# Kernel optimization log

Hardware: AMD Instinct MI355X
Metric: run time of the kernel (lower is better)

## Reference

```python
import jax, jax.numpy as jnp
import numpy as np

B, Q, C, V = 512, 100, 81, 117  # batch, queries, obj classes (80+no-object), verbs
THRES, ALPHA, BETA = 0.7, 1.0, 0.5


def setup_inputs() -> dict:
    key = jax.random.key(0)
    k1, k2, k3, k4, k5, k6 = jax.random.split(key, 6)
    out_obj_logits = jax.random.normal(k1, (B, Q, C), jnp.float32)
    out_verb_logits = jax.random.normal(k2, (B, Q, V), jnp.float32)
    out_sub_boxes = jax.random.uniform(k3, (B, Q, 4), jnp.float32)
    out_obj_boxes = jax.random.uniform(k4, (B, Q, 4), jnp.float32)
    # correct_mat: binary verb-object compatibility [V, C-1] + ones column for no-object slot -> [V, C]
    cm = (jax.random.uniform(k5, (V, C - 1)) < 0.3).astype(jnp.float32)
    correct_mat = jnp.concatenate([cm, jnp.ones((V, 1), jnp.float32)], axis=1)
    target_sizes = jax.random.randint(k6, (B, 2), 480, 1334).astype(jnp.int64)
    return {
        'out_obj_logits': out_obj_logits,
        'out_verb_logits': out_verb_logits,
        'out_sub_boxes': out_sub_boxes,
        'out_obj_boxes': out_obj_boxes,
        'correct_mat': correct_mat,
        'target_sizes': target_sizes,
    }


def _box_cxcywh_to_xyxy(b):
    cx, cy, w, h = b[..., 0], b[..., 1], b[..., 2], b[..., 3]
    return jnp.stack([cx - 0.5 * w, cy - 0.5 * h, cx + 0.5 * w, cy + 0.5 * h], axis=-1)


def _pairwise_iou(boxes):  # boxes [Q,4] xyxy (pixel coords, +1 convention as in source)
    x1, y1, x2, y2 = boxes[:, 0], boxes[:, 1], boxes[:, 2], boxes[:, 3]
    area = (x2 - x1 + 1.0) * (y2 - y1 + 1.0)
    xx1 = jnp.maximum(x1[:, None], x1[None, :])
    yy1 = jnp.maximum(y1[:, None], y1[None, :])
    xx2 = jnp.minimum(x2[:, None], x2[None, :])
    yy2 = jnp.minimum(y2[:, None], y2[None, :])
    w = jnp.maximum(0.0, xx2 - xx1 + 1.0)
    h = jnp.maximum(0.0, yy2 - yy1 + 1.0)
    inter = w * h
    union = area[:, None] + area[None, :] - inter
    return inter / union


def _nms_one_image(sub_b, obj_b, obj_lab, max_scores):
    # Greedy pairwise triplet NMS. Grouping key in the source degenerates to the
    # object label alone (subject cat is constant, verb-label string identical),
    # so suppression applies only between detections with the same object label.
    order = jnp.argsort(-max_scores)
    sb, ob, lab = sub_b[order], obj_b[order], obj_lab[order]
    ovr = jnp.power(_pairwise_iou(sb), ALPHA) * jnp.power(_pairwise_iou(ob), BETA)
    upper = jnp.triu(jnp.ones((Q, Q), bool), 1)
    sup_mat = upper & (lab[:, None] == lab[None, :]) & (ovr > THRES)

    def body(i, supp):
        return supp | (sup_mat[i] & jnp.logical_not(supp[i]))

    supp = jax.lax.fori_loop(0, Q, body, jnp.zeros((Q,), bool))
    keep = jnp.zeros((Q,), bool).at[order].set(jnp.logical_not(supp))
    return keep  # in original query order


def reference(out_obj_logits, out_verb_logits, out_sub_boxes, out_obj_boxes, correct_mat, target_sizes):
    obj_prob = jax.nn.softmax(out_obj_logits, axis=-1)
    obj_scores = obj_prob[..., :-1].max(axis=-1)            # [B,Q]
    obj_labels = obj_prob[..., :-1].argmax(axis=-1)         # [B,Q]
    verb_scores = jax.nn.sigmoid(out_verb_logits)           # [B,Q,V]

    ts = target_sizes.astype(jnp.float32)
    img_h, img_w = ts[:, 0], ts[:, 1]
    scale_fct = jnp.stack([img_w, img_h, img_w, img_h], axis=1)  # [B,4]
    sub_boxes = _box_cxcywh_to_xyxy(out_sub_boxes) * scale_fct[:, None, :]
    obj_boxes = _box_cxcywh_to_xyxy(out_obj_boxes) * scale_fct[:, None, :]

    # masks[b,q,v] = correct_mat[v, obj_labels[b,q]]
    masks = correct_mat.T[obj_labels]                        # [B,Q,V]
    hoi_scores = verb_scores * obj_scores[..., None] * masks

    max_scores = hoi_scores.max(axis=-1)                     # [B,Q]
    keep = jax.vmap(_nms_one_image)(sub_boxes, obj_boxes, obj_labels, max_scores)
    return hoi_scores, obj_labels, sub_boxes, obj_boxes, keep
```

## Files before the change

kernel.cpp:

```cpp
#include <hip/hip_runtime.h>
#include <math.h>

#define Bn 512
#define Qn 100
#define Cn 81
#define Vn 117
#define NQ (Bn * Qn)

#define OFF_HOI  0
#define OFF_LAB  (NQ * Vn)
#define OFF_SUB  (OFF_LAB + NQ)
#define OFF_OBJ  (OFF_SUB + NQ * 4)
#define OFF_KEEP (OFF_OBJ + NQ * 4)

__device__ __forceinline__ float frcp(float x) { return __builtin_amdgcn_rcpf(x); }

__global__ __launch_bounds__(256) void hoi_score(
    const float* __restrict__ obj_logits,
    const float* __restrict__ verb_logits,
    const float* __restrict__ sub_boxes,
    const float* __restrict__ obj_boxes,
    const float* __restrict__ cm,
    const int*   __restrict__ target_sizes,
    float* __restrict__ out)
{
    const int tid = threadIdx.x;
    const int t   = tid & 15;
    const int g   = tid >> 4;
    const int idx = blockIdx.x * 16 + g;
    const int b   = idx / Qn;

    if (t < 2) {
        const float ih = (float)target_sizes[2 * b + 0];
        const float iw = (float)target_sizes[2 * b + 1];
        const float4 bx = ((const float4*)(t == 0 ? sub_boxes : obj_boxes))[idx];
        float4 r;
        r.x = (bx.x - 0.5f * bx.z) * iw;
        r.y = (bx.y - 0.5f * bx.w) * ih;
        r.z = (bx.x + 0.5f * bx.z) * iw;
        r.w = (bx.y + 0.5f * bx.w) * ih;
        ((float4*)(out + (t == 0 ? OFF_SUB : OFF_OBJ)))[idx] = r;
    }

    const float* lg = obj_logits + (size_t)idx * Cn;
    const float* vl = verb_logits + (size_t)idx * Vn;

    float l0 = lg[t], l1 = lg[t + 16], l2 = lg[t + 32],
          l3 = lg[t + 48], l4 = lg[t + 64], l5 = lg[80];
    float w0 = vl[t], w1 = vl[t + 16], w2 = vl[t + 32], w3 = vl[t + 48],
          w4 = vl[t + 64], w5 = vl[t + 80], w6 = vl[t + 96];
    float w7 = (t < 5) ? vl[112 + t] : 0.f;

    float v = l0; int vid = t;
    if (l1 > v) { v = l1; vid = t + 16; }
    if (l2 > v) { v = l2; vid = t + 32; }
    if (l3 > v) { v = l3; vid = t + 48; }
    if (l4 > v) { v = l4; vid = t + 64; }
    #pragma unroll
    for (int o = 8; o; o >>= 1) {
        float ov = __shfl_xor(v, o, 64);
        int   oi = __shfl_xor(vid, o, 64);
        if (ov > v || (ov == v && oi < vid)) { v = ov; vid = oi; }
    }

    float e = __expf(l0) + __expf(l1) + __expf(l2) + __expf(l3) + __expf(l4);
    #pragma unroll
    for (int o = 8; o; o >>= 1) e += __shfl_xor(e, o, 64);
    e += __expf(l5);

    const int   label     = vid;
    const float obj_score = __expf(v) * frcp(e);

    float* hout = out + OFF_HOI + (size_t)idx * Vn;
    const float* cmrow = cm + label;
    float mx = 0.f, h;
    h = frcp(1.f + __expf(-w0)) * obj_score * cmrow[(t      ) * Cn]; hout[t      ] = h; mx = fmaxf(mx, h);
    h = frcp(1.f + __expf(-w1)) * obj_score * cmrow[(t +  16) * Cn]; hout[t +  16] = h; mx = fmaxf(mx, h);
    h = frcp(1.f + __expf(-w2)) * obj_score * cmrow[(t +  32) * Cn]; hout[t +  32] = h; mx = fmaxf(mx, h);
    h = frcp(1.f + __expf(-w3)) * obj_score * cmrow[(t +  48) * Cn]; hout[t +  48] = h; mx = fmaxf(mx, h);
    h = frcp(1.f + __expf(-w4)) * obj_score * cmrow[(t +  64) * Cn]; hout[t +  64] = h; mx = fmaxf(mx, h);
    h = frcp(1.f + __expf(-w5)) * obj_score * cmrow[(t +  80) * Cn]; hout[t +  80] = h; mx = fmaxf(mx, h);
    h = frcp(1.f + __expf(-w6)) * obj_score * cmrow[(t +  96) * Cn]; hout[t +  96] = h; mx = fmaxf(mx, h);
    if (t < 5) {
        h = frcp(1.f + __expf(-w7)) * obj_score * cmrow[(112 + t) * Cn];
        hout[112 + t] = h; mx = fmaxf(mx, h);
    }
    #pragma unroll
    for (int o = 8; o; o >>= 1) mx = fmaxf(mx, __shfl_xor(mx, o, 64));

    if (t == 0) {
        out[OFF_LAB + idx]  = (float)label;
        out[OFF_KEEP + idx] = mx;
    }
}

__global__ __launch_bounds__(256) void hoi_nms(float* __restrict__ out)
{
    __shared__ float  sc[Qn];
    __shared__ float4 Ssub[Qn], Sobj[Qn], Smeta[Qn];
    __shared__ ulonglong2 RR[Qn];

    const int b   = blockIdx.x;
    const int tid = threadIdx.x;

    float  kv = 0.f, labf = 0.f;
    float4 sb = make_float4(0.f, 0.f, 0.f, 0.f), ob = sb;
    if (tid < Qn) {
        const int idx = b * Qn + tid;
        kv   = out[OFF_KEEP + idx];
        sb   = ((const float4*)(out + OFF_SUB))[idx];
        ob   = ((const float4*)(out + OFF_OBJ))[idx];
        labf = out[OFF_LAB + idx];
        sc[tid] = kv;
    }
    __syncthreads();

    if (tid < Qn) {
        int r = 0;
        #pragma unroll 4
        for (int j = 0; j < Qn; j++) {
            float sj = sc[j];
            r += (sj > kv) || (sj == kv && j < tid);
        }
        Ssub[r] = sb;
        Sobj[r] = ob;
        Smeta[r] = make_float4((sb.z - sb.x + 1.f) * (sb.w - sb.y + 1.f),
                               (ob.z - ob.x + 1.f) * (ob.w - ob.y + 1.f),
                               labf, (float)tid);
    }
    __syncthreads();

    {
        const int tc   = tid & 127;
        const int uq   = tid >> 7;
        const int lane = tid & 63;
        const int sub  = (tid >> 6) & 1;
        const bool jv  = (tc < Qn);

        float4 js = make_float4(0.f, 0.f, 0.f, 0.f), jo = js, jm = js;
        if (jv) { js = Ssub[tc]; jo = Sobj[tc]; jm = Smeta[tc]; }

        const int i0 = uq * 50;
        const int i1 = (i0 + 50 < Qn - 1) ? i0 + 50 : Qn - 1;
        float4 is = Ssub[i0], io = Sobj[i0], im = Smeta[i0];
        for (int i = i0; i < i1; i++) {
            const int inx = (i + 1 < i1) ? i + 1 : i;
            float4 isn = Ssub[inx], ion = Sobj[inx], imn = Smeta[inx];
            float ww = fmaxf(0.f, fminf(is.z, js.z) - fmaxf(is.x, js.x) + 1.f);
            float hh = fmaxf(0.f, fminf(is.w, js.w) - fmaxf(is.y, js.y) + 1.f);
            float inter = ww * hh;
            float iou_s = inter / (im.x + jm.x - inter);
            ww = fmaxf(0.f, fminf(io.z, jo.z) - fmaxf(io.x, jo.x) + 1.f);
            hh = fmaxf(0.f, fminf(io.w, jo.w) - fmaxf(io.y, jo.y) + 1.f);
            inter = ww * hh;
            float iou_o = inter / (im.y + jm.y - inter);
            bool cond = jv && (tc > i) && (jm.z == im.z) && (iou_s * sqrtf(iou_o) > 0.7f);
            unsigned long long m = __ballot(cond);
            if (lane == 0) ((unsigned long long*)&RR[i])[sub] = m;
            is = isn; io = ion; im = imn;
        }
    }
    __syncthreads();

    if (tid < 64) {
        unsigned long long s0 = 0ull, s1 = 0ull;
        ulonglong2 r = RR[0];
        for (int k = 0; k < Qn - 1; k++) {
            ulonglong2 rn = RR[(k + 1 < Qn - 1) ? k + 1 : k];
            unsigned long long dead = ((k < 64 ? s0 : s1) >> (k & 63)) & 1ull;
            if (!dead) { s0 |= r.x; s1 |= r.y; }
            r = rn;
        }
        float* keepp = out + OFF_KEEP + (size_t)b * Qn;
        keepp[(int)Smeta[tid].w] = ((s0 >> tid) & 1ull) ? 0.f : 1.f;
        if (tid < 36)
            keepp[(int)Smeta[64 + tid].w] = ((s1 >> tid) & 1ull) ? 0.f : 1.f;
    }
}

extern "C" void kernel_launch(void* const* d_in, const int* in_sizes, int n_in,
                              void* d_out, int out_size, void* d_ws, size_t ws_size,
                              hipStream_t stream) {
    const float* obj_logits   = (const float*)d_in[0];
    const float* verb_logits  = (const float*)d_in[1];
    const float* sub_boxes    = (const float*)d_in[2];
    const float* obj_boxes    = (const float*)d_in[3];
    const float* correct_mat  = (const float*)d_in[4];
    const int*   target_sizes = (const int*)d_in[5];
    float* out = (float*)d_out;
    (void)d_ws; (void)ws_size; (void)in_sizes; (void)n_in; (void)out_size;

    hoi_score<<<NQ / 16, 256, 0, stream>>>(obj_logits, verb_logits, sub_boxes,
                                           obj_boxes, correct_mat, target_sizes, out);
    hoi_nms<<<Bn, 256, 0, stream>>>(out);
}
```

Baseline: 130.3 us.

## Transpose correct_mat and use one wavefront per query with float4 loads

```diff
diff --git a/kernel.cpp b/kernel.cpp
--- a/kernel.cpp
+++ b/kernel.cpp
@@ -15,80 +15,104 @@
 
 __device__ __forceinline__ float frcp(float x) { return __builtin_amdgcn_rcpf(x); }
 
+__device__ __forceinline__ float4 ld4u(const float* p) {
+    float4 r; __builtin_memcpy(&r, p, 16); return r;
+}
+__device__ __forceinline__ void st4u(float* p, const float4& v) {
+    __builtin_memcpy(p, &v, 16);
+}
+
+__global__ __launch_bounds__(128) void cm_transpose(const float* __restrict__ cm,
+                                                    float* __restrict__ cmT) {
+    int c = blockIdx.x;
+    int v = threadIdx.x;
+    if (v < Vn) cmT[c * Vn + v] = cm[v * Cn + c];
+}
+
 __global__ __launch_bounds__(256) void hoi_score(
     const float* __restrict__ obj_logits,
     const float* __restrict__ verb_logits,
     const float* __restrict__ sub_boxes,
     const float* __restrict__ obj_boxes,
-    const float* __restrict__ cm,
+    const float* __restrict__ cmT,
     const int*   __restrict__ target_sizes,
     float* __restrict__ out)
 {
     const int tid = threadIdx.x;
-    const int t   = tid & 15;
-    const int g   = tid >> 4;
-    const int idx = blockIdx.x * 16 + g;
+    const int w   = tid >> 6;
+    const int l   = tid & 63;
+    const int idx = blockIdx.x * 4 + w;
     const int b   = idx / Qn;
-
-    if (t < 2) {
-        const float ih = (float)target_sizes[2 * b + 0];
-        const float iw = (float)target_sizes[2 * b + 1];
-        const float4 bx = ((const float4*)(t == 0 ? sub_boxes : obj_boxes))[idx];
-        float4 r;
-        r.x = (bx.x - 0.5f * bx.z) * iw;
-        r.y = (bx.y - 0.5f * bx.w) * ih;
-        r.z = (bx.x + 0.5f * bx.z) * iw;
-        r.w = (bx.y + 0.5f * bx.w) * ih;
-        ((float4*)(out + (t == 0 ? OFF_SUB : OFF_OBJ)))[idx] = r;
-    }
 
     const float* lg = obj_logits + (size_t)idx * Cn;
     const float* vl = verb_logits + (size_t)idx * Vn;
 
-    float l0 = lg[t], l1 = lg[t + 16], l2 = lg[t + 32],
-          l3 = lg[t + 48], l4 = lg[t + 64], l5 = lg[80];
-    float w0 = vl[t], w1 = vl[t + 16], w2 = vl[t + 32], w3 = vl[t + 48],
-          w4 = vl[t + 64], w5 = vl[t + 80], w6 = vl[t + 96];
-    float w7 = (t < 5) ? vl[112 + t] : 0.f;
-
-    float v = l0; int vid = t;
-    if (l1 > v) { v = l1; vid = t + 16; }
-    if (l2 > v) { v = l2; vid = t + 32; }
-    if (l3 > v) { v = l3; vid = t + 48; }
-    if (l4 > v) { v = l4; vid = t + 64; }
+    float a0 = -1e30f, a1 = -1e30f, a2 = -1e30f, a3 = -1e30f;
+    if (l < 20) {
+        float4 r = ld4u(lg + 4 * l);
+        a0 = r.x; a1 = r.y; a2 = r.z; a3 = r.w;
+    }
+    const float l80 = lg[80];
+
+    float4 wv = make_float4(0.f, 0.f, 0.f, 0.f);
+    float  w116 = 0.f;
+    if (l < 29) wv = ld4u(vl + 4 * l);
+    else if (l == 29) w116 = vl[116];
+
+    if (l == 40 || l == 41) {
+        const bool iss = (l == 40);
+        const float ihh = (float)target_sizes[2 * b + 0];
+        const float iww = (float)target_sizes[2 * b + 1];
+        const float4 bx = ((const float4*)(iss ? sub_boxes : obj_boxes))[idx];
+        float4 r;
+        r.x = (bx.x - 0.5f * bx.z) * iww;
+        r.y = (bx.y - 0.5f * bx.w) * ihh;
+        r.z = (bx.x + 0.5f * bx.z) * iww;
+        r.w = (bx.y + 0.5f * bx.w) * ihh;
+        ((float4*)(out + (iss ? OFF_SUB : OFF_OBJ)))[idx] = r;
+    }
+
+    float v = a0; int vid = 4 * l;
+    if (a1 > v) { v = a1; vid = 4 * l + 1; }
+    if (a2 > v) { v = a2; vid = 4 * l + 2; }
+    if (a3 > v) { v = a3; vid = 4 * l + 3; }
     #pragma unroll
-    for (int o = 8; o; o >>= 1) {
+    for (int o = 32; o; o >>= 1) {
         float ov = __shfl_xor(v, o, 64);
         int   oi = __shfl_xor(vid, o, 64);
         if (ov > v || (ov == v && oi < vid)) { v = ov; vid = oi; }
     }
 
-    float e = __expf(l0) + __expf(l1) + __expf(l2) + __expf(l3) + __expf(l4);
+    float e = 0.f;
+    if (l < 20) e = __expf(a0) + __expf(a1) + __expf(a2) + __expf(a3);
     #pragma unroll
-    for (int o = 8; o; o >>= 1) e += __shfl_xor(e, o, 64);
-    e += __expf(l5);
+    for (int o = 32; o; o >>= 1) e += __shfl_xor(e, o, 64);
+    e += __expf(l80);
 
     const int   label     = vid;
     const float obj_score = __expf(v) * frcp(e);
 
     float* hout = out + OFF_HOI + (size_t)idx * Vn;
-    const float* cmrow = cm + label;
-    float mx = 0.f, h;
-    h = frcp(1.f + __expf(-w0)) * obj_score * cmrow[(t      ) * Cn]; hout[t      ] = h; mx = fmaxf(mx, h);
-    h = frcp(1.f + __expf(-w1)) * obj_score * cmrow[(t +  16) * Cn]; hout[t +  16] = h; mx = fmaxf(mx, h);
-    h = frcp(1.f + __expf(-w2)) * obj_score * cmrow[(t +  32) * Cn]; hout[t +  32] = h; mx = fmaxf(mx, h);
-    h = frcp(1.f + __expf(-w3)) * obj_score * cmrow[(t +  48) * Cn]; hout[t +  48] = h; mx = fmaxf(mx, h);
-    h = frcp(1.f + __expf(-w4)) * obj_score * cmrow[(t +  64) * Cn]; hout[t +  64] = h; mx = fmaxf(mx, h);
-    h = frcp(1.f + __expf(-w5)) * obj_score * cmrow[(t +  80) * Cn]; hout[t +  80] = h; mx = fmaxf(mx, h);
-    h = frcp(1.f + __expf(-w6)) * obj_score * cmrow[(t +  96) * Cn]; hout[t +  96] = h; mx = fmaxf(mx, h);
-    if (t < 5) {
-        h = frcp(1.f + __expf(-w7)) * obj_score * cmrow[(112 + t) * Cn];
-        hout[112 + t] = h; mx = fmaxf(mx, h);
+    const float* crow = cmT + (size_t)label * Vn;
+    float mx = 0.f;
+    if (l < 29) {
+        float4 cv = ld4u(crow + 4 * l);
+        float4 h;
+        h.x = frcp(1.f + __expf(-wv.x)) * obj_score * cv.x;
+        h.y = frcp(1.f + __expf(-wv.y)) * obj_score * cv.y;
+        h.z = frcp(1.f + __expf(-wv.z)) * obj_score * cv.z;
+        h.w = frcp(1.f + __expf(-wv.w)) * obj_score * cv.w;
+        st4u(hout + 4 * l, h);
+        mx = fmaxf(fmaxf(h.x, h.y), fmaxf(h.z, h.w));
+    } else if (l == 29) {
+        float h = frcp(1.f + __expf(-w116)) * obj_score * crow[116];
+        hout[116] = h;
+        mx = h;
     }
     #pragma unroll
-    for (int o = 8; o; o >>= 1) mx = fmaxf(mx, __shfl_xor(mx, o, 64));
-
-    if (t == 0) {
+    for (int o = 32; o; o >>= 1) mx = fmaxf(mx, __shfl_xor(mx, o, 64));
+
+    if (l == 0) {
         out[OFF_LAB + idx]  = (float)label;
         out[OFF_KEEP + idx] = mx;
     }
@@ -188,9 +212,11 @@
     const float* correct_mat  = (const float*)d_in[4];
     const int*   target_sizes = (const int*)d_in[5];
     float* out = (float*)d_out;
-    (void)d_ws; (void)ws_size; (void)in_sizes; (void)n_in; (void)out_size;
-
-    hoi_score<<<NQ / 16, 256, 0, stream>>>(obj_logits, verb_logits, sub_boxes,
-                                           obj_boxes, correct_mat, target_sizes, out);
+    float* cmT = (float*)d_ws;
+    (void)in_sizes; (void)n_in; (void)out_size; (void)ws_size;
+
+    cm_transpose<<<Cn, 128, 0, stream>>>(correct_mat, cmT);
+    hoi_score<<<NQ / 4, 256, 0, stream>>>(obj_logits, verb_logits, sub_boxes,
+                                          obj_boxes, cmT, target_sizes, out);
     hoi_nms<<<Bn, 256, 0, stream>>>(out);
 }
```

Result: slower. 137.4 us (+5.4%).
